# Kernel tuning notes

Measured on AMD Instinct MI355X. Metric: run time of the kernel, lower is better.

Reference implementation:

```python
import jax, jax.numpy as jnp
import numpy as np

N, E, D_IN, HID, HEADS, TS_OUT = 100000, 200000, 165, 64, 8, 5
HD1 = HID // HEADS  # 8 per-head channels in layer 1
HD2 = HID           # 64 per-head channels in layer 2 (concat=False -> mean)


def _glorot(key, shape):
    fan_in, fan_out = shape[0], shape[1]
    s = np.sqrt(6.0 / (fan_in + fan_out)).astype(np.float32)
    return jax.random.uniform(key, shape, jnp.float32, -s, s)


def setup_inputs() -> dict:
    key = jax.random.key(0)
    ks = jax.random.split(key, 24)
    inp = {
        "x": jax.random.normal(ks[0], (N, D_IN), jnp.float32),
        "edge_index": jax.random.randint(ks[1], (2, E), 0, N, jnp.int32),
        "timestamp_target": jax.random.randint(ks[2], (N,), 0, TS_OUT, jnp.int32),
        "node_target": jax.random.randint(ks[3], (N,), 0, 2, jnp.int32),
        "node_mask": jax.random.randint(ks[4], (N,), 0, 2, jnp.int32).astype(jnp.bool_),
        # GATConv layer 1: in=165 -> 8 heads x 8 ch, concat -> 64
        "W1": _glorot(ks[5], (D_IN, HEADS * HD1)),
        "att_src1": _glorot(ks[6], (HEADS, HD1)),
        "att_dst1": _glorot(ks[7], (HEADS, HD1)),
        "b1": jnp.zeros((HEADS * HD1,), jnp.float32),
        # GATConv layer 2: in=64 -> 8 heads x 64 ch, mean -> 64
        "W2": _glorot(ks[8], (HID, HEADS * HD2)),
        "att_src2": _glorot(ks[9], (HEADS, HD2)),
        "att_dst2": _glorot(ks[10], (HEADS, HD2)),
        "b2": jnp.zeros((HD2,), jnp.float32),
        # timestamp predictor MLP
        "ts_w1": _glorot(ks[11], (HID, HID)), "ts_b1": jnp.zeros((HID,), jnp.float32),
        "ts_w2": _glorot(ks[12], (HID, TS_OUT)), "ts_b2": jnp.zeros((TS_OUT,), jnp.float32),
        # class predictor MLP
        "cls_w1": _glorot(ks[13], (HID, HID)), "cls_b1": jnp.zeros((HID,), jnp.float32),
        "cls_w2": _glorot(ks[14], (HID, 2)), "cls_b2": jnp.zeros((2,), jnp.float32),
    }
    return inp


def _gat_layer(x, src, dst, n, W, a_src, a_dst, b, concat):
    H, C = a_src.shape
    h = (x @ W).reshape(n, H, C)                      # [N,H,C]
    a_s = (h * a_src).sum(-1)                         # [N,H]
    a_d = (h * a_dst).sum(-1)                         # [N,H]
    alpha = jax.nn.leaky_relu(a_s[src] + a_d[dst], 0.2)   # [E,H]
    amax = jax.ops.segment_max(alpha, dst, num_segments=n)
    ea = jnp.exp(alpha - amax[dst])
    denom = jax.ops.segment_sum(ea, dst, num_segments=n)
    a = ea / (denom[dst] + 1e-16)                     # segment softmax over incoming edges
    out = jax.ops.segment_sum(h[src] * a[:, :, None], dst, num_segments=n)  # [N,H,C]
    out = out.reshape(n, H * C) if concat else out.mean(axis=1)
    return out + b


def _ce(logits, targets):
    lp = jax.nn.log_softmax(logits, axis=-1)
    return -jnp.take_along_axis(lp, targets[:, None].astype(jnp.int32), axis=1)[:, 0]


def reference(x, edge_index, timestamp_target, node_target, node_mask,
              W1, att_src1, att_dst1, b1, W2, att_src2, att_dst2, b2,
              ts_w1, ts_b1, ts_w2, ts_b2, cls_w1, cls_b1, cls_w2, cls_b2):
    n = x.shape[0]
    loops = jnp.arange(n, dtype=edge_index.dtype)
    src = jnp.concatenate([edge_index[0], loops])     # add self loops (PyG default)
    dst = jnp.concatenate([edge_index[1], loops])
    h = _gat_layer(x, src, dst, n, W1, att_src1, att_dst1, b1, True)   # [N,64]
    h = _gat_layer(h, src, dst, n, W2, att_src2, att_dst2, b2, False)  # [N,64]
    # gradient reversal is identity in the forward pass
    ts_pred = jax.nn.relu(h @ ts_w1 + ts_b1) @ ts_w2 + ts_b2           # [N,5]
    cls_pred = jax.nn.relu(h @ cls_w1 + cls_b1) @ cls_w2 + cls_b2      # [N,2]
    ts_loss = _ce(ts_pred, timestamp_target).mean()
    m = node_mask.astype(jnp.float32)
    cls_loss = (_ce(cls_pred, node_target) * m).sum() / m.sum()
    return cls_loss + 1.0 * ts_loss
```

## Files before the change

### kernel.cpp

```cpp
#include <hip/hip_runtime.h>
#include <hip/hip_bf16.h>

#define NN 100000
#define NE 200000
#define NT (NE + NN)
#define DIN 165
#define PREPB 128
#define INITB 391
#define PACKB 32
#define W1PB 24
#define MISCGRID (PREPB + INITB + PACKB + W1PB)
#define NODEB 1563
#define XDW ((size_t)NN * DIN)
#define G1ROWS 32
#define G1NDMA 21

typedef __attribute__((ext_vector_type(8))) short bf16x8_t;
typedef __attribute__((ext_vector_type(4))) float f32x4_t;
typedef _Float16 h2_t __attribute__((ext_vector_type(2)));
typedef _Float16 f16x8_t __attribute__((ext_vector_type(8)));

#define AS1 __attribute__((address_space(1)))
#define AS3 __attribute__((address_space(3)))

static __device__ __forceinline__ unsigned short f2bf(float f) {
    __hip_bfloat16 b = __float2bfloat16(f);
    return *(unsigned short*)&b;
}
static __device__ __forceinline__ float bfu(unsigned short u) {
    __hip_bfloat16 b = *(__hip_bfloat16*)&u;
    return __bfloat162float(b);
}
static __device__ __forceinline__ unsigned pkh2(float a, float b) {
    h2_t v; v[0] = (_Float16)a; v[1] = (_Float16)b;
    return *(unsigned*)&v;
}


__global__ __launch_bounds__(256) void k_misc(const float* W2, const float* a2s, const float* a2d,
                                              float* wsd, __hip_bfloat16* W2pT,
                                              int* cnt, int* fill,
                                              const float* tsw1, const float* cw1,
                                              __hip_bfloat16* wB,
                                              const float* W1, unsigned* W1pT, float* zbuf) {
    int b = blockIdx.x;
    int tid = threadIdx.x;
    if (b < PREPB) {
        int i = b * 256 + tid;
        int c = i >> 9, j = i & 511;
        int hh = j >> 6, kk = j & 63;
        W2pT[i] = __float2bfloat16(W2[kk * 512 + hh * 64 + c]);
        if (b == 0) zbuf[tid] = 0.f;
        if (i < 512) {
            int h = i >> 6, k = i & 63;
            float s = 0.f, d = 0.f;
            for (int cc = 0; cc < 64; cc++) {
                float w = W2[k * 512 + h * 64 + cc];
                s += w * a2s[h * 64 + cc];
                d += w * a2d[h * 64 + cc];
            }
            wsd[i] = s; wsd[512 + i] = d;
        }
    } else if (b < PREPB + INITB) {
        int i = (b - PREPB) * 256 + tid;
        if (i < NN) { cnt[i] = 0; fill[i] = 0; }
    } else if (b < PREPB + INITB + PACKB) {
        int i = (b - PREPB - INITB) * 256 + tid;
        if (i < 8192) {
            int c = i >> 6, k = i & 63;
            float v = (c < 64) ? tsw1[k * 64 + c] : cw1[k * 64 + (c - 64)];
            wB[i] = __float2bfloat16(v);
        }
    } else {
        int i = (b - PREPB - INITB - PACKB) * 256 + tid;
        if (i < 6144) {
            int c = i / 96, kp = i - c * 96;
            int k = 2 * kp;
            float f0 = (k < DIN) ? W1[k * 64 + c] : 0.f;
            float f1 = (k + 1 < DIN) ? W1[(k + 1) * 64 + c] : 0.f;
            W1pT[i] = pkh2(f0, f1);
        }
    }
}


__global__ __launch_bounds__(256) void k_count(const int* dstE, int* cnt) {
    int e = blockIdx.x * 256 + threadIdx.x;
    if (e < NE) atomicAdd(&cnt[dstE[e]], 1);
}

__global__ __launch_bounds__(256) void k_scanA(const int* cnt, int* rowptr, int* bsum) {
    __shared__ int sm[256];
    int t = threadIdx.x;
    int base = blockIdx.x * 1024;
    int v[4]; int s = 0;
    for (int i = 0; i < 4; i++) {
        int idx = base + t * 4 + i;
        v[i] = (idx < NN) ? (cnt[idx] + 1) : 0;
        s += v[i];
    }
    sm[t] = s; __syncthreads();
    for (int off = 1; off < 256; off <<= 1) {
        int x = (t >= off) ? sm[t - off] : 0;
        __syncthreads();
        sm[t] += x;
        __syncthreads();
    }
    int run = sm[t] - s;
    for (int i = 0; i < 4; i++) {
        run += v[i];
        int idx = base + t * 4 + i;
        if (idx < NN) rowptr[idx + 1] = run;
    }
    if (t == 255) bsum[blockIdx.x] = sm[255];
}

__global__ __launch_bounds__(64) void k_scanB(int* bsum, int nb) {
    int lane = threadIdx.x;
    int v0 = (lane < nb) ? bsum[lane] : 0;
    int v1 = (64 + lane < nb) ? bsum[64 + lane] : 0;
    int s0 = v0;
    for (int off = 1; off < 64; off <<= 1) { int t = __shfl_up(s0, off); if (lane >= off) s0 += t; }
    int tot0 = __shfl(s0, 63);
    int s1 = v1;
    for (int off = 1; off < 64; off <<= 1) { int t = __shfl_up(s1, off); if (lane >= off) s1 += t; }
    if (lane < nb) bsum[lane] = s0 - v0;
    if (64 + lane < nb) bsum[64 + lane] = tot0 + s1 - v1;
}

__global__ __launch_bounds__(256) void k_scanC(const int* bsum, int* rowptr) {
    int i = blockIdx.x * 256 + threadIdx.x;
    if (i < NN) rowptr[i + 1] += bsum[i >> 10];
    if (i == 0) rowptr[0] = 0;
}

__global__ __launch_bounds__(256) void k_fill(const int* srcE, const int* dstE,
                                              const int* rowptr, int* fill, int* col, int* rowv) {
    int i = blockIdx.x * 256 + threadIdx.x;
    if (i >= NT) return;
    int s, d;
    if (i < NE) { s = srcE[i]; d = dstE[i]; }
    else        { s = i - NE; d = s; }
    int p = rowptr[d] + atomicAdd(&fill[d], 1);
    col[p] = s;
    rowv[p] = d;
}


__global__ __launch_bounds__(128) void k_gemm1(const float* x, const unsigned* W1pT,
                                               const float* att_s, const float* att_d,
                                               const float* zsrc,
                                               __hip_bfloat16* h1b, float* aad1) {
    __shared__ float X[G1NDMA * 256];
    int tid = threadIdx.x;
    int l = tid & 63, w = tid >> 6;
    int n0 = blockIdx.x * G1ROWS;
    int frow = l & 15, kg = l >> 4;

    size_t tb = (size_t)n0 * DIN;
    for (int i = w; i < G1NDMA; i += 2) {
        size_t gd = tb + (size_t)i * 256 + (size_t)l * 4;
        const float* g = (gd + 4 <= XDW) ? (x + gd) : (zsrc + l * 4);
        __builtin_amdgcn_global_load_lds((const AS1 float*)g,
                                         (AS3 float*)(X + i * 256), 16, 0, 0);
    }
    uint4 B[6][4];
    #pragma unroll
    for (int s = 0; s < 6; s++)
        #pragma unroll
        for (int t = 0; t < 4; t++)
            B[s][t] = *(const uint4*)&W1pT[(t * 16 + frow) * 96 + s * 16 + kg * 4];
    __syncthreads();

    f32x4_t acc[4] = {};
    int rbase = (w * 16 + frow) * DIN + kg * 8;
    #pragma unroll
    for (int s = 0; s < 6; s++) {
        f16x8_t av;
        #pragma unroll
        for (int j = 0; j < 8; j++) av[j] = (_Float16)X[rbase + s * 32 + j];
        #pragma unroll
        for (int t = 0; t < 4; t++)
            acc[t] = __builtin_amdgcn_mfma_f32_16x16x32_f16(av, *(f16x8_t*)&B[s][t], acc[t], 0, 0, 0);
    }

    int nw = n0 + w * 16;
    float asv[4], adv[4];
    #pragma unroll
    for (int t = 0; t < 4; t++) {
        int c = t * 16 + frow;
        asv[t] = att_s[c]; adv[t] = att_d[c];
    }
    int hb = (l >> 3) & 1;
    #pragma unroll
    for (int q = 0; q < 4; q++) {
        int n = nw + kg * 4 + q;
        #pragma unroll
        for (int t = 0; t < 4; t++) {
            float sv = acc[t][q] * asv[t];
            float dv = acc[t][q] * adv[t];
            sv += __shfl_xor(sv, 1); sv += __shfl_xor(sv, 2); sv += __shfl_xor(sv, 4);
            dv += __shfl_xor(dv, 1); dv += __shfl_xor(dv, 2); dv += __shfl_xor(dv, 4);
            if ((l & 7) == 0) {
                int h = t * 2 + hb;
                aad1[(size_t)n * 16 + h]     = sv;
                aad1[(size_t)n * 16 + 8 + h] = dv;
            }
        }
    }

    __syncthreads();
    unsigned short* Hw = (unsigned short*)X + w * 1152;
    #pragma unroll
    for (int t = 0; t < 4; t++)
        #pragma unroll
        for (int q = 0; q < 4; q++)
            Hw[(kg * 4 + q) * 72 + t * 16 + frow] = f2bf(acc[t][q]);
    int rr = l >> 2, cc = l & 3;
    int n2 = nw + rr;
    unsigned short* dst = (unsigned short*)h1b + (size_t)n2 * 64 + cc * 16;
    *(uint4*)dst       = *(const uint4*)&Hw[rr * 72 + cc * 16];
    *(uint4*)(dst + 8) = *(const uint4*)&Hw[rr * 72 + cc * 16 + 8];
}


__global__ __launch_bounds__(256) void k_edgew(const float* aad, const int* col, const int* rowv,
                                               __hip_bfloat16* web) {
    int e = blockIdx.x * 256 + threadIdx.x;
    if (e >= NT) return;
    int s = col[e], d = rowv[e];
    float4 s0 = *(const float4*)&aad[(size_t)s * 16];
    float4 s1 = *(const float4*)&aad[(size_t)s * 16 + 4];
    float4 dd0 = *(const float4*)&aad[(size_t)d * 16 + 8];
    float4 dd1 = *(const float4*)&aad[(size_t)d * 16 + 12];
    float as[8] = {s0.x, s0.y, s0.z, s0.w, s1.x, s1.y, s1.z, s1.w};
    float ad[8] = {dd0.x, dd0.y, dd0.z, dd0.w, dd1.x, dd1.y, dd1.z, dd1.w};
    unsigned p[4];
    #pragma unroll
    for (int q = 0; q < 4; q++) {
        float a0 = as[2*q]   + ad[2*q];
        float a1 = as[2*q+1] + ad[2*q+1];
        a0 = a0 > 0.f ? a0 : 0.2f * a0;
        a1 = a1 > 0.f ? a1 : 0.2f * a1;
        p[q] = (unsigned)f2bf(__expf(a0)) | ((unsigned)f2bf(__expf(a1)) << 16);
    }
    *(uint4*)&web[(size_t)e * 8] = make_uint4(p[0], p[1], p[2], p[3]);
}


__global__ __launch_bounds__(256) void k_agg1f(const __hip_bfloat16* h1b, const __hip_bfloat16* we1b,
                                               const int* rowptr, const int* col,
                                               const float* b1, const float* wsd,
                                               __hip_bfloat16* out1b, float* aad2) {
    int tid = threadIdx.x;
    int q = tid & 15;
    int n = blockIdx.x * 16 + (tid >> 4);
    int hq = q >> 1;
    const unsigned short* h1u = (const unsigned short*)h1b;
    const unsigned short* weu = (const unsigned short*)we1b;
    int rs = rowptr[n], re = rowptr[n + 1];
    float acc0 = 0.f, acc1 = 0.f, acc2 = 0.f, acc3 = 0.f, den = 0.f;
    for (int eb = rs; eb < re; eb += 4) {
        int c4[4];
        #pragma unroll
        for (int j = 0; j < 4; j++) c4[j] = col[min(eb + j, re - 1)];
        #pragma unroll
        for (int j = 0; j < 4; j++) {
            int e = min(eb + j, re - 1);
            float wv = bfu(weu[(size_t)e * 8 + hq]);
            wv = (eb + j < re) ? wv : 0.f;
            uint2 hv = *(const uint2*)&h1u[(size_t)c4[j] * 64 + q * 4];
            den  += wv;
            acc0 += wv * bfu((unsigned short)(hv.x & 0xffff));
            acc1 += wv * bfu((unsigned short)(hv.x >> 16));
            acc2 += wv * bfu((unsigned short)(hv.y & 0xffff));
            acc3 += wv * bfu((unsigned short)(hv.y >> 16));
        }
    }
    float4 bb = *(const float4*)&b1[q * 4];
    float dd = den + 1e-16f;
    unsigned short u0 = f2bf(acc0 / dd + bb.x);
    unsigned short u1 = f2bf(acc1 / dd + bb.y);
    unsigned short u2 = f2bf(acc2 / dd + bb.z);
    unsigned short u3 = f2bf(acc3 / dd + bb.w);
    unsigned short* ou = (unsigned short*)out1b;
    *(uint2*)&ou[(size_t)n * 64 + q * 4] =
        make_uint2((unsigned)u0 | ((unsigned)u1 << 16), (unsigned)u2 | ((unsigned)u3 << 16));

    float r0 = bfu(u0), r1 = bfu(u1), r2 = bfu(u2), r3 = bfu(u3);
    float p[16];
    #pragma unroll
    for (int j = 0; j < 16; j++) {
        float4 wv = *(const float4*)&wsd[j * 64 + q * 4];
        p[j] = r0 * wv.x + r1 * wv.y + r2 * wv.z + r3 * wv.w;
    }
    #pragma unroll
    for (int s = 1; s < 16; s <<= 1)
        #pragma unroll
        for (int j = 0; j < 16; j++) p[j] += __shfl_xor(p[j], s);
    float myp = 0.f;
    #pragma unroll
    for (int j = 0; j < 16; j++) myp = (q == j) ? p[j] : myp;
    aad2[(size_t)n * 16 + q] = myp;
}


__global__ __launch_bounds__(256) void k_l2f(const __hip_bfloat16* out1b, const __hip_bfloat16* we2b,
                                             const int* rowptr, const int* col,
                                             const __hip_bfloat16* W2pT, const float* b2,
                                             const __hip_bfloat16* wB,
                                             const float* tsb1, const float* cb1,
                                             const float* tsw2, const float* tsb2,
                                             const float* cw2, const float* cb2,
                                             const int* tst, const int* ctg, const unsigned char* msk,
                                             float* part) {
    __shared__ unsigned short Ax[64 * 512];
    __shared__ unsigned short Bl[64 * 72];
    __shared__ float red[4][3];
    int tid = threadIdx.x;
    int l = tid & 63, w = tid >> 6;
    int n0 = blockIdx.x * 64;
    int frow = l & 15, kg = l >> 4;

    const unsigned short* o1u = (const unsigned short*)out1b;
    const unsigned short* weu = (const unsigned short*)we2b;
    int q4 = tid & 15;
    #pragma unroll 1
    for (int pass = 0; pass < 4; pass++) {
        int j = pass * 16 + (tid >> 4);
        int n = n0 + j;
        int rs = 0, re = 0;
        if (n < NN) { rs = rowptr[n]; re = rowptr[n + 1]; }
        float acc[8][4];
        float den[8];
        #pragma unroll
        for (int h = 0; h < 8; h++) {
            den[h] = 0.f;
            #pragma unroll
            for (int c = 0; c < 4; c++) acc[h][c] = 0.f;
        }
        for (int eb = rs; eb < re; eb += 4) {
            int c4[4];
            #pragma unroll
            for (int jj = 0; jj < 4; jj++) c4[jj] = col[min(eb + jj, re - 1)];
            #pragma unroll
            for (int jj = 0; jj < 4; jj++) {
                int e = min(eb + jj, re - 1);
                uint4 wv = *(const uint4*)&weu[(size_t)e * 8];
                uint2 hv = *(const uint2*)&o1u[(size_t)c4[jj] * 64 + q4 * 4];
                float vm = (eb + jj < re) ? 1.f : 0.f;
                float hc0 = bfu((unsigned short)(hv.x & 0xffff));
                float hc1 = bfu((unsigned short)(hv.x >> 16));
                float hc2 = bfu((unsigned short)(hv.y & 0xffff));
                float hc3 = bfu((unsigned short)(hv.y >> 16));
                float wt[8] = {bfu((unsigned short)(wv.x & 0xffff)), bfu((unsigned short)(wv.x >> 16)),
                               bfu((unsigned short)(wv.y & 0xffff)), bfu((unsigned short)(wv.y >> 16)),
                               bfu((unsigned short)(wv.z & 0xffff)), bfu((unsigned short)(wv.z >> 16)),
                               bfu((unsigned short)(wv.w & 0xffff)), bfu((unsigned short)(wv.w >> 16))};
                #pragma unroll
                for (int h = 0; h < 8; h++) {
                    float ww = wt[h] * vm;
                    den[h] += ww;
                    acc[h][0] += ww * hc0;
                    acc[h][1] += ww * hc1;
                    acc[h][2] += ww * hc2;
                    acc[h][3] += ww * hc3;
                }
            }
        }
        #pragma unroll
        for (int h = 0; h < 8; h++) {
            float dd = den[h] + 1e-16f;
            unsigned lo = (unsigned)f2bf(acc[h][0] / dd) | ((unsigned)f2bf(acc[h][1] / dd) << 16);
            unsigned hi = (unsigned)f2bf(acc[h][2] / dd) | ((unsigned)f2bf(acc[h][3] / dd) << 16);
            int blk = (h * 8 + (q4 >> 1)) ^ (j & 7);
            *(uint2*)&Ax[j * 512 + blk * 8 + (q4 & 1) * 4] = make_uint2(lo, hi);
        }
    }
    __syncthreads();

    const unsigned short* B_g = (const unsigned short*)W2pT;
    f32x4_t gacc[4] = {};
    #pragma unroll 1
    for (int k0 = 0; k0 < 512; k0 += 64) {
        #pragma unroll
        for (int ll = 0; ll < 2; ll++) {
            int u = tid + ll * 256;
            int r = u >> 3, seg = u & 7;
            *(uint4*)&Bl[r * 72 + seg * 8] = *(const uint4*)&B_g[(size_t)r * 512 + k0 + seg * 8];
        }
        __syncthreads();
        #pragma unroll
        for (int kk = 0; kk < 2; kk++) {
            int blk = ((k0 >> 3) + kk * 4 + kg) ^ (frow & 7);
            bf16x8_t a = *(const bf16x8_t*)&Ax[(w * 16 + frow) * 512 + blk * 8];
            #pragma unroll
            for (int t = 0; t < 4; t++) {
                bf16x8_t bb = *(const bf16x8_t*)&Bl[(t * 16 + frow) * 72 + kk * 32 + kg * 8];
                gacc[t] = __builtin_amdgcn_mfma_f32_16x16x32_bf16(a, bb, gacc[t], 0, 0, 0);
            }
        }
        __syncthreads();
    }

    unsigned short* o2L = Ax;
    #pragma unroll
    for (int t = 0; t < 4; t++) {
        float bias = b2[t * 16 + frow];
        #pragma unroll
        for (int q = 0; q < 4; q++)
            o2L[(w * 16 + kg * 4 + q) * 72 + t * 16 + frow] = f2bf(0.125f * gacc[t][q] + bias);
    }
    __syncthreads();
    const unsigned short* wBu = (const unsigned short*)wB;
    f32x4_t a2c[8] = {};
    #pragma unroll
    for (int kk = 0; kk < 2; kk++) {
        bf16x8_t a2 = *(const bf16x8_t*)&o2L[(w * 16 + frow) * 72 + kk * 32 + kg * 8];
        #pragma unroll
        for (int t2 = 0; t2 < 8; t2++) {
            bf16x8_t b2f = *(const bf16x8_t*)&wBu[(t2 * 16 + frow) * 64 + kk * 32 + kg * 8];
            a2c[t2] = __builtin_amdgcn_mfma_f32_16x16x32_bf16(a2, b2f, a2c[t2], 0, 0, 0);
        }
    }

    float lg[4][5]; float lc[4][2];
    #pragma unroll
    for (int q = 0; q < 4; q++) {
        #pragma unroll
        for (int t = 0; t < 5; t++) lg[q][t] = 0.f;
        lc[q][0] = 0.f; lc[q][1] = 0.f;
    }
    #pragma unroll
    for (int t2 = 0; t2 < 4; t2++) {
        int c = t2 * 16 + frow;
        float bb = tsb1[c];
        float w0 = tsw2[c * 5 + 0], w1 = tsw2[c * 5 + 1], w2 = tsw2[c * 5 + 2],
              w3 = tsw2[c * 5 + 3], w4 = tsw2[c * 5 + 4];
        #pragma unroll
        for (int q = 0; q < 4; q++) {
            float v = fmaxf(a2c[t2][q] + bb, 0.f);
            lg[q][0] += v * w0; lg[q][1] += v * w1; lg[q][2] += v * w2;
            lg[q][3] += v * w3; lg[q][4] += v * w4;
        }
    }
    #pragma unroll
    for (int t2 = 0; t2 < 4; t2++) {
        int c = t2 * 16 + frow;
        float bb = cb1[c];
        float u0 = cw2[c * 2], u1 = cw2[c * 2 + 1];
        #pragma unroll
        for (int q = 0; q < 4; q++) {
            float v = fmaxf(a2c[t2 + 4][q] + bb, 0.f);
            lc[q][0] += v * u0; lc[q][1] += v * u1;
        }
    }
    #pragma unroll
    for (int q = 0; q < 4; q++) {
        #pragma unroll
        for (int t = 0; t < 5; t++) {
            lg[q][t] += __shfl_xor(lg[q][t], 1);
            lg[q][t] += __shfl_xor(lg[q][t], 2);
            lg[q][t] += __shfl_xor(lg[q][t], 4);
            lg[q][t] += __shfl_xor(lg[q][t], 8);
        }
        #pragma unroll
        for (int t = 0; t < 2; t++) {
            lc[q][t] += __shfl_xor(lc[q][t], 1);
            lc[q][t] += __shfl_xor(lc[q][t], 2);
            lc[q][t] += __shfl_xor(lc[q][t], 4);
            lc[q][t] += __shfl_xor(lc[q][t], 8);
        }
    }
    float tsl = 0.f, cll = 0.f, mval = 0.f;
    if (frow == 0) {
        #pragma unroll
        for (int q = 0; q < 4; q++) {
            int n = n0 + w * 16 + kg * 4 + q;
            if (n < NN) {
                float L[5];
                #pragma unroll
                for (int t = 0; t < 5; t++) L[t] = lg[q][t] + tsb2[t];
                float mx = fmaxf(fmaxf(fmaxf(L[0], L[1]), fmaxf(L[2], L[3])), L[4]);
                float se = 0.f;
                #pragma unroll
                for (int t = 0; t < 5; t++) se += __expf(L[t] - mx);
                int tg = tst[n];
                float pick = 0.f;
                #pragma unroll
                for (int t = 0; t < 5; t++) pick += (t == tg) ? L[t] : 0.f;
                tsl += mx + __logf(se) - pick;
                float C0 = lc[q][0] + cb2[0];
                float C1 = lc[q][1] + cb2[1];
                float mx2 = fmaxf(C0, C1);
                float lse2 = mx2 + __logf(__expf(C0 - mx2) + __expf(C1 - mx2));
                float mv = msk[n] ? 1.f : 0.f;
                float pick2 = ctg[n] ? C1 : C0;
                cll += (lse2 - pick2) * mv;
                mval += mv;
            }
        }
    }
    #pragma unroll
    for (int off = 1; off < 64; off <<= 1) {
        tsl  += __shfl_xor(tsl, off);
        cll  += __shfl_xor(cll, off);
        mval += __shfl_xor(mval, off);
    }
    if (l == 0) { red[w][0] = tsl; red[w][1] = cll; red[w][2] = mval; }
    __syncthreads();
    if (tid == 0) {
        part[blockIdx.x * 3 + 0] = red[0][0] + red[1][0] + red[2][0] + red[3][0];
        part[blockIdx.x * 3 + 1] = red[0][1] + red[1][1] + red[2][1] + red[3][1];
        part[blockIdx.x * 3 + 2] = red[0][2] + red[1][2] + red[2][2] + red[3][2];
    }
}

__global__ __launch_bounds__(256) void k_final(const float* part, float* out, int nb) {
    __shared__ float sm[3][256];
    int tid = threadIdx.x;
    float a = 0, b = 0, c = 0;
    for (int i = tid; i < nb; i += 256) { a += part[i*3]; b += part[i*3+1]; c += part[i*3+2]; }
    sm[0][tid] = a; sm[1][tid] = b; sm[2][tid] = c;
    __syncthreads();
    for (int s = 128; s > 0; s >>= 1) {
        if (tid < s) {
            sm[0][tid] += sm[0][tid + s];
            sm[1][tid] += sm[1][tid + s];
            sm[2][tid] += sm[2][tid + s];
        }
        __syncthreads();
    }
    if (tid == 0) out[0] = sm[1][0] / sm[2][0] + sm[0][0] / (float)NN;
}


extern "C" void kernel_launch(void* const* d_in, const int* in_sizes, int n_in,
                              void* d_out, int out_size, void* d_ws, size_t ws_size,
                              hipStream_t stream) {
    const float* x    = (const float*)d_in[0];
    const int*   ei   = (const int*)d_in[1];
    const int*   tst  = (const int*)d_in[2];
    const int*   ctg  = (const int*)d_in[3];
    const unsigned char* msk = (const unsigned char*)d_in[4];
    const float* W1   = (const float*)d_in[5];
    const float* a1s  = (const float*)d_in[6];
    const float* a1d  = (const float*)d_in[7];
    const float* b1   = (const float*)d_in[8];
    const float* W2   = (const float*)d_in[9];
    const float* a2s  = (const float*)d_in[10];
    const float* a2d  = (const float*)d_in[11];
    const float* b2   = (const float*)d_in[12];
    const float* tsw1 = (const float*)d_in[13];
    const float* tsb1 = (const float*)d_in[14];
    const float* tsw2 = (const float*)d_in[15];
    const float* tsb2 = (const float*)d_in[16];
    const float* cw1  = (const float*)d_in[17];
    const float* cb1  = (const float*)d_in[18];
    const float* cw2  = (const float*)d_in[19];
    const float* cb2  = (const float*)d_in[20];
    const int* srcE = ei;
    const int* dstE = ei + NE;

    char* ws = (char*)d_ws;
    size_t off = 0;
    auto alloc = [&](size_t b) { size_t o = off; off = (off + b + 255) & ~(size_t)255; return o; };
    int*   cnt    = (int*)(ws + alloc((size_t)NN * 4));
    int*   fill   = (int*)(ws + alloc((size_t)NN * 4));
    int*   rowptr = (int*)(ws + alloc((size_t)(NN + 1) * 4));
    int*   bsum   = (int*)(ws + alloc(128 * 4));
    int*   col    = (int*)(ws + alloc((size_t)NT * 4));
    int*   rowv   = (int*)(ws + alloc((size_t)NT * 4));
    float* aad1   = (float*)(ws + alloc((size_t)NN * 16 * 4));
    __hip_bfloat16* out1b = (__hip_bfloat16*)(ws + alloc((size_t)NN * 64 * 2));
    float* aad2   = (float*)(ws + alloc((size_t)NN * 16 * 4));
    float* wsd    = (float*)(ws + alloc(1024 * 4));
    __hip_bfloat16* W2pT  = (__hip_bfloat16*)(ws + alloc(32768 * 2));
    __hip_bfloat16* wB    = (__hip_bfloat16*)(ws + alloc(8192 * 2));
    unsigned* W1pT = (unsigned*)(ws + alloc(6144 * 4));
    float* zbuf   = (float*)(ws + alloc(256 * 4));
    __hip_bfloat16* h1b   = (__hip_bfloat16*)(ws + alloc((size_t)NN * 64 * 2));
    __hip_bfloat16* web   = (__hip_bfloat16*)(ws + alloc((size_t)NT * 8 * 2));
    float* part   = (float*)(ws + alloc((size_t)NODEB * 3 * 4));
    (void)ws_size; (void)in_sizes; (void)n_in; (void)out_size;

    int nb_scan = (NN + 1023) / 1024;

    k_misc<<<MISCGRID, 256, 0, stream>>>(W2, a2s, a2d, wsd, W2pT, cnt, fill,
                                         tsw1, cw1, wB, W1, W1pT, zbuf);
    k_count<<<(NE + 255) / 256, 256, 0, stream>>>(dstE, cnt);
    k_scanA<<<nb_scan, 256, 0, stream>>>(cnt, rowptr, bsum);
    k_scanB<<<1, 64, 0, stream>>>(bsum, nb_scan);
    k_scanC<<<(NN + 255) / 256, 256, 0, stream>>>(bsum, rowptr);
    k_fill<<<(NT + 255) / 256, 256, 0, stream>>>(srcE, dstE, rowptr, fill, col, rowv);

    k_gemm1<<<NN / G1ROWS, 128, 0, stream>>>(x, W1pT, a1s, a1d, zbuf, h1b, aad1);
    k_edgew<<<(NT + 255) / 256, 256, 0, stream>>>(aad1, col, rowv, web);
    k_agg1f<<<NN / 16, 256, 0, stream>>>(h1b, web, rowptr, col, b1, wsd, out1b, aad2);
    k_edgew<<<(NT + 255) / 256, 256, 0, stream>>>(aad2, col, rowv, web);

    k_l2f<<<NODEB, 256, 0, stream>>>(out1b, web, rowptr, col, W2pT, b2, wB,
                                     tsb1, cb1, tsw2, tsb2, cw2, cb2, tst, ctg, msk, part);

    k_final<<<1, 256, 0, stream>>>(part, (float*)d_out, NODEB);
}
```

Before: 198.7 us.

## Double k_l2f block to 512 threads and split MFMA and MLP work across waves

Raises the fused layer-2 kernel from 256 to 512 threads per block. Aggregation now runs in 2 passes instead of 4, the GEMM output tiles are split between wave pairs, and the timestamp and class MLP heads go to separate wave groups. The aim is more latency hiding in the gather-heavy aggregation and less serial MFMA work per wave. The division is also replaced by a reciprocal multiply. The block already uses about 73 KB of LDS, so occupancy in blocks stays the same. The larger block means more threads per CU, at the risk of register pressure under the 512 launch bound.

```diff
diff --git a/kernel.cpp b/kernel.cpp
--- a/kernel.cpp
+++ b/kernel.cpp
@@ -305,7 +305,7 @@
 }
 
 
-__global__ __launch_bounds__(256) void k_l2f(const __hip_bfloat16* out1b, const __hip_bfloat16* we2b,
+__global__ __launch_bounds__(512) void k_l2f(const __hip_bfloat16* out1b, const __hip_bfloat16* we2b,
                                              const int* rowptr, const int* col,
                                              const __hip_bfloat16* W2pT, const float* b2,
                                              const __hip_bfloat16* wB,
@@ -316,7 +316,7 @@
                                              float* part) {
     __shared__ unsigned short Ax[64 * 512];
     __shared__ unsigned short Bl[64 * 72];
-    __shared__ float red[4][3];
+    __shared__ float red[8][3];
     int tid = threadIdx.x;
     int l = tid & 63, w = tid >> 6;
     int n0 = blockIdx.x * 64;
@@ -326,8 +326,8 @@
     const unsigned short* weu = (const unsigned short*)we2b;
     int q4 = tid & 15;
     #pragma unroll 1
-    for (int pass = 0; pass < 4; pass++) {
-        int j = pass * 16 + (tid >> 4);
+    for (int pass = 0; pass < 2; pass++) {
+        int j = pass * 32 + (tid >> 4);
         int n = n0 + j;
         int rs = 0, re = 0;
         if (n < NN) { rs = rowptr[n]; re = rowptr[n + 1]; }
@@ -370,9 +370,9 @@
         }
         #pragma unroll
         for (int h = 0; h < 8; h++) {
-            float dd = den[h] + 1e-16f;
-            unsigned lo = (unsigned)f2bf(acc[h][0] / dd) | ((unsigned)f2bf(acc[h][1] / dd) << 16);
-            unsigned hi = (unsigned)f2bf(acc[h][2] / dd) | ((unsigned)f2bf(acc[h][3] / dd) << 16);
+            float inv = 1.0f / (den[h] + 1e-16f);
+            unsigned lo = (unsigned)f2bf(acc[h][0] * inv) | ((unsigned)f2bf(acc[h][1] * inv) << 16);
+            unsigned hi = (unsigned)f2bf(acc[h][2] * inv) | ((unsigned)f2bf(acc[h][3] * inv) << 16);
             int blk = (h * 8 + (q4 >> 1)) ^ (j & 7);
             *(uint2*)&Ax[j * 512 + blk * 8 + (q4 & 1) * 4] = make_uint2(lo, hi);
         }
@@ -380,23 +380,23 @@
     __syncthreads();
 
     const unsigned short* B_g = (const unsigned short*)W2pT;
-    f32x4_t gacc[4] = {};
+    int r0 = (w & 3) * 16;
+    int c0 = (w >> 2) * 32;
+    f32x4_t gacc[2] = {};
     #pragma unroll 1
     for (int k0 = 0; k0 < 512; k0 += 64) {
-        #pragma unroll
-        for (int ll = 0; ll < 2; ll++) {
-            int u = tid + ll * 256;
-            int r = u >> 3, seg = u & 7;
+        {
+            int r = tid >> 3, seg = tid & 7;
             *(uint4*)&Bl[r * 72 + seg * 8] = *(const uint4*)&B_g[(size_t)r * 512 + k0 + seg * 8];
         }
         __syncthreads();
         #pragma unroll
         for (int kk = 0; kk < 2; kk++) {
             int blk = ((k0 >> 3) + kk * 4 + kg) ^ (frow & 7);
-            bf16x8_t a = *(const bf16x8_t*)&Ax[(w * 16 + frow) * 512 + blk * 8];
-            #pragma unroll
-            for (int t = 0; t < 4; t++) {
-                bf16x8_t bb = *(const bf16x8_t*)&Bl[(t * 16 + frow) * 72 + kk * 32 + kg * 8];
+            bf16x8_t a = *(const bf16x8_t*)&Ax[(r0 + frow) * 512 + blk * 8];
+            #pragma unroll
+            for (int t = 0; t < 2; t++) {
+                bf16x8_t bb = *(const bf16x8_t*)&Bl[(c0 + t * 16 + frow) * 72 + kk * 32 + kg * 8];
                 gacc[t] = __builtin_amdgcn_mfma_f32_16x16x32_bf16(a, bb, gacc[t], 0, 0, 0);
             }
         }
@@ -405,99 +405,115 @@
 
     unsigned short* o2L = Ax;
     #pragma unroll
-    for (int t = 0; t < 4; t++) {
-        float bias = b2[t * 16 + frow];
+    for (int t = 0; t < 2; t++) {
+        float bias = b2[c0 + t * 16 + frow];
+        f32x4_t g = gacc[t];
         #pragma unroll
         for (int q = 0; q < 4; q++)
-            o2L[(w * 16 + kg * 4 + q) * 72 + t * 16 + frow] = f2bf(0.125f * gacc[t][q] + bias);
+            o2L[(r0 + kg * 4 + q) * 72 + c0 + t * 16 + frow] = f2bf(0.125f * g[q] + bias);
     }
     __syncthreads();
     const unsigned short* wBu = (const unsigned short*)wB;
-    f32x4_t a2c[8] = {};
+    int m0 = (w & 3) * 16;
+    int h0 = (w >> 2) * 64;
+    f32x4_t a2c[4] = {};
     #pragma unroll
     for (int kk = 0; kk < 2; kk++) {
-        bf16x8_t a2 = *(const bf16x8_t*)&o2L[(w * 16 + frow) * 72 + kk * 32 + kg * 8];
-        #pragma unroll
-        for (int t2 = 0; t2 < 8; t2++) {
-            bf16x8_t b2f = *(const bf16x8_t*)&wBu[(t2 * 16 + frow) * 64 + kk * 32 + kg * 8];
-            a2c[t2] = __builtin_amdgcn_mfma_f32_16x16x32_bf16(a2, b2f, a2c[t2], 0, 0, 0);
-        }
-    }
-
-    float lg[4][5]; float lc[4][2];
-    #pragma unroll
-    for (int q = 0; q < 4; q++) {
-        #pragma unroll
-        for (int t = 0; t < 5; t++) lg[q][t] = 0.f;
-        lc[q][0] = 0.f; lc[q][1] = 0.f;
-    }
-    #pragma unroll
-    for (int t2 = 0; t2 < 4; t2++) {
-        int c = t2 * 16 + frow;
-        float bb = tsb1[c];
-        float w0 = tsw2[c * 5 + 0], w1 = tsw2[c * 5 + 1], w2 = tsw2[c * 5 + 2],
-              w3 = tsw2[c * 5 + 3], w4 = tsw2[c * 5 + 4];
-        #pragma unroll
-        for (int q = 0; q < 4; q++) {
-            float v = fmaxf(a2c[t2][q] + bb, 0.f);
-            lg[q][0] += v * w0; lg[q][1] += v * w1; lg[q][2] += v * w2;
-            lg[q][3] += v * w3; lg[q][4] += v * w4;
-        }
-    }
-    #pragma unroll
-    for (int t2 = 0; t2 < 4; t2++) {
-        int c = t2 * 16 + frow;
-        float bb = cb1[c];
-        float u0 = cw2[c * 2], u1 = cw2[c * 2 + 1];
-        #pragma unroll
-        for (int q = 0; q < 4; q++) {
-            float v = fmaxf(a2c[t2 + 4][q] + bb, 0.f);
-            lc[q][0] += v * u0; lc[q][1] += v * u1;
-        }
-    }
-    #pragma unroll
-    for (int q = 0; q < 4; q++) {
-        #pragma unroll
-        for (int t = 0; t < 5; t++) {
-            lg[q][t] += __shfl_xor(lg[q][t], 1);
-            lg[q][t] += __shfl_xor(lg[q][t], 2);
-            lg[q][t] += __shfl_xor(lg[q][t], 4);
-            lg[q][t] += __shfl_xor(lg[q][t], 8);
-        }
-        #pragma unroll
-        for (int t = 0; t < 2; t++) {
-            lc[q][t] += __shfl_xor(lc[q][t], 1);
-            lc[q][t] += __shfl_xor(lc[q][t], 2);
-            lc[q][t] += __shfl_xor(lc[q][t], 4);
-            lc[q][t] += __shfl_xor(lc[q][t], 8);
-        }
-    }
+        bf16x8_t a2 = *(const bf16x8_t*)&o2L[(m0 + frow) * 72 + kk * 32 + kg * 8];
+        #pragma unroll
+        for (int t2 = 0; t2 < 4; t2++) {
+            bf16x8_t bf = *(const bf16x8_t*)&wBu[(h0 + t2 * 16 + frow) * 64 + kk * 32 + kg * 8];
+            a2c[t2] = __builtin_amdgcn_mfma_f32_16x16x32_bf16(a2, bf, a2c[t2], 0, 0, 0);
+        }
+    }
+
     float tsl = 0.f, cll = 0.f, mval = 0.f;
-    if (frow == 0) {
-        #pragma unroll
-        for (int q = 0; q < 4; q++) {
-            int n = n0 + w * 16 + kg * 4 + q;
-            if (n < NN) {
-                float L[5];
-                #pragma unroll
-                for (int t = 0; t < 5; t++) L[t] = lg[q][t] + tsb2[t];
-                float mx = fmaxf(fmaxf(fmaxf(L[0], L[1]), fmaxf(L[2], L[3])), L[4]);
-                float se = 0.f;
-                #pragma unroll
-                for (int t = 0; t < 5; t++) se += __expf(L[t] - mx);
-                int tg = tst[n];
-                float pick = 0.f;
-                #pragma unroll
-                for (int t = 0; t < 5; t++) pick += (t == tg) ? L[t] : 0.f;
-                tsl += mx + __logf(se) - pick;
-                float C0 = lc[q][0] + cb2[0];
-                float C1 = lc[q][1] + cb2[1];
-                float mx2 = fmaxf(C0, C1);
-                float lse2 = mx2 + __logf(__expf(C0 - mx2) + __expf(C1 - mx2));
-                float mv = msk[n] ? 1.f : 0.f;
-                float pick2 = ctg[n] ? C1 : C0;
-                cll += (lse2 - pick2) * mv;
-                mval += mv;
+    if ((w >> 2) == 0) {
+        float lg[4][5];
+        #pragma unroll
+        for (int q = 0; q < 4; q++)
+            #pragma unroll
+            for (int t = 0; t < 5; t++) lg[q][t] = 0.f;
+        #pragma unroll
+        for (int t2 = 0; t2 < 4; t2++) {
+            int c = t2 * 16 + frow;
+            float bb = tsb1[c];
+            float w0 = tsw2[c * 5 + 0], w1 = tsw2[c * 5 + 1], w2 = tsw2[c * 5 + 2],
+                  w3 = tsw2[c * 5 + 3], w4 = tsw2[c * 5 + 4];
+            #pragma unroll
+            for (int q = 0; q < 4; q++) {
+                float v = fmaxf(a2c[t2][q] + bb, 0.f);
+                lg[q][0] += v * w0; lg[q][1] += v * w1; lg[q][2] += v * w2;
+                lg[q][3] += v * w3; lg[q][4] += v * w4;
+            }
+        }
+        #pragma unroll
+        for (int q = 0; q < 4; q++)
+            #pragma unroll
+            for (int t = 0; t < 5; t++) {
+                lg[q][t] += __shfl_xor(lg[q][t], 1);
+                lg[q][t] += __shfl_xor(lg[q][t], 2);
+                lg[q][t] += __shfl_xor(lg[q][t], 4);
+                lg[q][t] += __shfl_xor(lg[q][t], 8);
+            }
+        if (frow == 0) {
+            #pragma unroll
+            for (int q = 0; q < 4; q++) {
+                int n = n0 + m0 + kg * 4 + q;
+                if (n < NN) {
+                    float L[5];
+                    #pragma unroll
+                    for (int t = 0; t < 5; t++) L[t] = lg[q][t] + tsb2[t];
+                    float mx = fmaxf(fmaxf(fmaxf(L[0], L[1]), fmaxf(L[2], L[3])), L[4]);
+                    float se = 0.f;
+                    #pragma unroll
+                    for (int t = 0; t < 5; t++) se += __expf(L[t] - mx);
+                    int tg = tst[n];
+                    float pick = 0.f;
+                    #pragma unroll
+                    for (int t = 0; t < 5; t++) pick += (t == tg) ? L[t] : 0.f;
+                    tsl += mx + __logf(se) - pick;
+                }
+            }
+        }
+    } else {
+        float lc[4][2];
+        #pragma unroll
+        for (int q = 0; q < 4; q++) { lc[q][0] = 0.f; lc[q][1] = 0.f; }
+        #pragma unroll
+        for (int t2 = 0; t2 < 4; t2++) {
+            int c = t2 * 16 + frow;
+            float bb = cb1[c];
+            float u0 = cw2[c * 2], u1 = cw2[c * 2 + 1];
+            #pragma unroll
+            for (int q = 0; q < 4; q++) {
+                float v = fmaxf(a2c[t2][q] + bb, 0.f);
+                lc[q][0] += v * u0; lc[q][1] += v * u1;
+            }
+        }
+        #pragma unroll
+        for (int q = 0; q < 4; q++)
+            #pragma unroll
+            for (int t = 0; t < 2; t++) {
+                lc[q][t] += __shfl_xor(lc[q][t], 1);
+                lc[q][t] += __shfl_xor(lc[q][t], 2);
+                lc[q][t] += __shfl_xor(lc[q][t], 4);
+                lc[q][t] += __shfl_xor(lc[q][t], 8);
+            }
+        if (frow == 0) {
+            #pragma unroll
+            for (int q = 0; q < 4; q++) {
+                int n = n0 + m0 + kg * 4 + q;
+                if (n < NN) {
+                    float C0 = lc[q][0] + cb2[0];
+                    float C1 = lc[q][1] + cb2[1];
+                    float mx2 = fmaxf(C0, C1);
+                    float lse2 = mx2 + __logf(__expf(C0 - mx2) + __expf(C1 - mx2));
+                    float mv = msk[n] ? 1.f : 0.f;
+                    float pick2 = ctg[n] ? C1 : C0;
+                    cll += (lse2 - pick2) * mv;
+                    mval += mv;
+                }
             }
         }
     }
@@ -510,9 +526,12 @@
     if (l == 0) { red[w][0] = tsl; red[w][1] = cll; red[w][2] = mval; }
     __syncthreads();
     if (tid == 0) {
-        part[blockIdx.x * 3 + 0] = red[0][0] + red[1][0] + red[2][0] + red[3][0];
-        part[blockIdx.x * 3 + 1] = red[0][1] + red[1][1] + red[2][1] + red[3][1];
-        part[blockIdx.x * 3 + 2] = red[0][2] + red[1][2] + red[2][2] + red[3][2];
+        float s0 = 0.f, s1 = 0.f, s2 = 0.f;
+        #pragma unroll
+        for (int ww = 0; ww < 8; ww++) { s0 += red[ww][0]; s1 += red[ww][1]; s2 += red[ww][2]; }
+        part[blockIdx.x * 3 + 0] = s0;
+        part[blockIdx.x * 3 + 1] = s1;
+        part[blockIdx.x * 3 + 2] = s2;
     }
 }
 
@@ -599,7 +618,7 @@
     k_agg1f<<<NN / 16, 256, 0, stream>>>(h1b, web, rowptr, col, b1, wsd, out1b, aad2);
     k_edgew<<<(NT + 255) / 256, 256, 0, stream>>>(aad2, col, rowv, web);
 
-    k_l2f<<<NODEB, 256, 0, stream>>>(out1b, web, rowptr, col, W2pT, b2, wB,
+    k_l2f<<<NODEB, 512, 0, stream>>>(out1b, web, rowptr, col, W2pT, b2, wB,
                                      tsb1, cb1, tsw2, tsb2, cw2, cb2, tst, ctg, msk, part);
 
     k_final<<<1, 256, 0, stream>>>(part, (float*)d_out, NODEB);
```

Result: slower. 209.5 us (+5.5%).
